# Optimization experiments

Hardware: AMD Instinct MI355X
Metric: run time of the kernel (lower is better)

The kernel has to match this reference:

```python
import jax, jax.numpy as jnp
import numpy as np


def setup_inputs() -> dict:
    key = jax.random.key(0)
    N, D = 8192, 16384  # tokens x latent dim
    inputs = jax.random.normal(key, (N, D), dtype=jnp.float32)
    return {"inputs": inputs, "k": 64}


def reference(inputs, k):
    # top-k along last axis, then scatter values into a zero tensor
    values, indices = jax.lax.top_k(inputs, k)          # [N, k]
    rows = jnp.arange(inputs.shape[0])[:, None]          # [N, 1]
    sparse = jnp.zeros_like(inputs).at[rows, indices].set(values)
    return sparse
```

## Files before the change

kernel.cpp:

```cpp
#include <hip/hip_runtime.h>

#define BLOCK 256
#define ROW_D 16384
#define VPT (ROW_D / (BLOCK * 4))

__device__ __forceinline__ unsigned keyOf(float f) {
    unsigned u = __float_as_uint(f);
    return (u & 0x80000000u) ? ~u : (u | 0x80000000u);
}
__device__ __forceinline__ float valOf(unsigned m) {
    unsigned u = (m & 0x80000000u) ? (m & 0x7FFFFFFFu) : ~m;
    return __uint_as_float(u);
}

__global__ __launch_bounds__(BLOCK, 4)
void TopKActivation_68324339745162_kernel(const float* __restrict__ in,
                                          float* __restrict__ out,
                                          const int* __restrict__ kptr) {
    __shared__ unsigned hist[256 * 32];
    __shared__ unsigned S[256];
    __shared__ unsigned sDigit, sGreater, sBinCnt, sBase;

    const int t = threadIdx.x;
    const unsigned cpy = (unsigned)t & 31u;
    const size_t rowOff = (size_t)blockIdx.x * (size_t)ROW_D;
    const float4* inRow = reinterpret_cast<const float4*>(in + rowOff);
    float4* outRow = reinterpret_cast<float4*>(out + rowOff);

    uint4 keys[VPT];
#pragma unroll
    for (int j = 0; j < VPT; ++j) {
        float4 v = inRow[t + BLOCK * j];
        keys[j].x = keyOf(v.x);
        keys[j].y = keyOf(v.y);
        keys[j].z = keyOf(v.z);
        keys[j].w = keyOf(v.w);
    }

    unsigned rank = (unsigned)(*kptr);
    unsigned prefix = 0u, pmask = 0u;

    for (int pass = 0; pass < 4; ++pass) {
        const int shift = 24 - 8 * pass;
        for (int i = t; i < 256 * 32; i += BLOCK) hist[i] = 0u;
        __syncthreads();
#pragma unroll
        for (int j = 0; j < VPT; ++j) {
            unsigned kk;
            kk = keys[j].x;
            if ((kk & pmask) == prefix) atomicAdd(&hist[(((kk >> shift) & 255u) << 5) | cpy], 1u);
            kk = keys[j].y;
            if ((kk & pmask) == prefix) atomicAdd(&hist[(((kk >> shift) & 255u) << 5) | cpy], 1u);
            kk = keys[j].z;
            if ((kk & pmask) == prefix) atomicAdd(&hist[(((kk >> shift) & 255u) << 5) | cpy], 1u);
            kk = keys[j].w;
            if ((kk & pmask) == prefix) atomicAdd(&hist[(((kk >> shift) & 255u) << 5) | cpy], 1u);
        }
        __syncthreads();
        unsigned c = 0u;
#pragma unroll
        for (int i = 0; i < 32; ++i) c += hist[((unsigned)t << 5) | (unsigned)((t + i) & 31)];
        S[t] = c;
        __syncthreads();
        for (int step = 1; step < 256; step <<= 1) {
            unsigned v = (t + step < 256) ? S[t + step] : 0u;
            __syncthreads();
            c += v;
            S[t] = c;
            __syncthreads();
        }
        unsigned Snext = (t < 255) ? S[t + 1] : 0u;
        if (c >= rank && Snext < rank) {
            sDigit   = (unsigned)t;
            sGreater = Snext;
            sBinCnt  = c - Snext;
        }
        __syncthreads();
        rank -= sGreater;
        prefix |= sDigit << shift;
        pmask  |= 255u << shift;
    }

    const unsigned T = prefix;
    const unsigned need = rank;
    const bool fastTies = (sBinCnt == need);

    if (fastTies) {
#pragma unroll
        for (int j = 0; j < VPT; ++j) {
            float4 o;
            o.x = (keys[j].x >= T) ? valOf(keys[j].x) : 0.0f;
            o.y = (keys[j].y >= T) ? valOf(keys[j].y) : 0.0f;
            o.z = (keys[j].z >= T) ? valOf(keys[j].z) : 0.0f;
            o.w = (keys[j].w >= T) ? valOf(keys[j].w) : 0.0f;
            outRow[t + BLOCK * j] = o;
        }
    } else {
        if (t == 0) sBase = 0u;
        for (int j = 0; j < VPT; ++j) {
            unsigned lc = (unsigned)(keys[j].x == T) + (unsigned)(keys[j].y == T) +
                          (unsigned)(keys[j].z == T) + (unsigned)(keys[j].w == T);
            __syncthreads();
            S[t] = lc;
            __syncthreads();
            unsigned run = lc;
            for (int step = 1; step < 256; step <<= 1) {
                unsigned v = (t >= step) ? S[t - step] : 0u;
                __syncthreads();
                run += v;
                S[t] = run;
                __syncthreads();
            }
            unsigned r = run - lc + sBase;
            float4 o;
            {
                unsigned kk = keys[j].x;
                if (kk > T) o.x = valOf(kk);
                else if (kk == T) { o.x = (r < need) ? valOf(kk) : 0.0f; ++r; }
                else o.x = 0.0f;
            }
            {
                unsigned kk = keys[j].y;
                if (kk > T) o.y = valOf(kk);
                else if (kk == T) { o.y = (r < need) ? valOf(kk) : 0.0f; ++r; }
                else o.y = 0.0f;
            }
            {
                unsigned kk = keys[j].z;
                if (kk > T) o.z = valOf(kk);
                else if (kk == T) { o.z = (r < need) ? valOf(kk) : 0.0f; ++r; }
                else o.z = 0.0f;
            }
            {
                unsigned kk = keys[j].w;
                if (kk > T) o.w = valOf(kk);
                else if (kk == T) { o.w = (r < need) ? valOf(kk) : 0.0f; ++r; }
                else o.w = 0.0f;
            }
            outRow[t + BLOCK * j] = o;
            __syncthreads();
            if (t == BLOCK - 1) sBase += run;
        }
    }
}

extern "C" void kernel_launch(void* const* d_in, const int* in_sizes, int n_in,
                              void* d_out, int out_size, void* d_ws, size_t ws_size,
                              hipStream_t stream) {
    const float* in = (const float*)d_in[0];
    const int* kptr = (const int*)d_in[1];
    float* out = (float*)d_out;
    const int N = in_sizes[0] / ROW_D;
    TopKActivation_68324339745162_kernel<<<dim3(N), dim3(BLOCK), 0, stream>>>(in, out, kptr);
}
```

Before: 890.5 us.

## Prefilter top-k candidates by per-thread max threshold, shrink histogram copies, wave-level scan

```diff
diff --git a/kernel.cpp b/kernel.cpp
--- a/kernel.cpp
+++ b/kernel.cpp
@@ -3,6 +3,8 @@
 #define BLOCK 256
 #define ROW_D 16384
 #define VPT (ROW_D / (BLOCK * 4))
+#define NC 8
+#define CAP 4096
 
 __device__ __forceinline__ unsigned keyOf(float f) {
     unsigned u = __float_as_uint(f);
@@ -11,23 +13,47 @@
 __device__ __forceinline__ float valOf(unsigned m) {
     unsigned u = (m & 0x80000000u) ? (m & 0x7FFFFFFFu) : ~m;
     return __uint_as_float(u);
+}
+
+__device__ __forceinline__ void waveFind(const unsigned* S, unsigned rank, int l,
+                                         unsigned* dDigit, unsigned* dGreater,
+                                         unsigned* dBinCnt) {
+    uint4 h = *reinterpret_cast<const uint4*>(S + 4 * l);
+    unsigned s3 = h.w;
+    unsigned s2 = h.z + s3;
+    unsigned s1 = h.y + s2;
+    unsigned s0 = h.x + s1;
+    unsigned inc = s0;
+#pragma unroll
+    for (int off = 1; off < 64; off <<= 1) {
+        unsigned v = __shfl_down(inc, off);
+        if (l + off < 64) inc += v;
+    }
+    const unsigned E = inc - s0;
+    const unsigned su0 = s0 + E, su1 = s1 + E, su2 = s2 + E, su3 = s3 + E, su4 = E;
+    if (su0 >= rank && su1 < rank) { *dDigit = 4u * l + 0u; *dGreater = su1; *dBinCnt = su0 - su1; }
+    if (su1 >= rank && su2 < rank) { *dDigit = 4u * l + 1u; *dGreater = su2; *dBinCnt = su1 - su2; }
+    if (su2 >= rank && su3 < rank) { *dDigit = 4u * l + 2u; *dGreater = su3; *dBinCnt = su2 - su3; }
+    if (su3 >= rank && su4 < rank) { *dDigit = 4u * l + 3u; *dGreater = su4; *dBinCnt = su3 - su4; }
 }
 
 __global__ __launch_bounds__(BLOCK, 4)
 void TopKActivation_68324339745162_kernel(const float* __restrict__ in,
                                           float* __restrict__ out,
                                           const int* __restrict__ kptr) {
-    __shared__ unsigned hist[256 * 32];
-    __shared__ unsigned S[256];
-    __shared__ unsigned sDigit, sGreater, sBinCnt, sBase;
+    __shared__ unsigned hist[256 * NC];
+    __shared__ __align__(16) unsigned S[256];
+    __shared__ unsigned cand[CAP];
+    __shared__ unsigned sDigit, sGreater, sBinCnt, sCnt, sBase;
 
     const int t = threadIdx.x;
-    const unsigned cpy = (unsigned)t & 31u;
+    const unsigned cpy = (unsigned)t & (NC - 1u);
     const size_t rowOff = (size_t)blockIdx.x * (size_t)ROW_D;
     const float4* inRow = reinterpret_cast<const float4*>(in + rowOff);
     float4* outRow = reinterpret_cast<float4*>(out + rowOff);
 
     uint4 keys[VPT];
+    unsigned mx = 0u;
 #pragma unroll
     for (int j = 0; j < VPT; ++j) {
         float4 v = inRow[t + BLOCK * j];
@@ -35,50 +61,81 @@
         keys[j].y = keyOf(v.y);
         keys[j].z = keyOf(v.z);
         keys[j].w = keyOf(v.w);
-    }
-
-    unsigned rank = (unsigned)(*kptr);
-    unsigned prefix = 0u, pmask = 0u;
-
+        unsigned a = keys[j].x > keys[j].y ? keys[j].x : keys[j].y;
+        unsigned b = keys[j].z > keys[j].w ? keys[j].z : keys[j].w;
+        a = a > b ? a : b;
+        mx = mx > a ? mx : a;
+    }
+
+    const unsigned k0 = (unsigned)(*kptr);
+    const bool screenOK = (k0 >= 1u && k0 <= (unsigned)BLOCK);
+
+    for (int i = t; i < 256 * NC; i += BLOCK) hist[i] = 0u;
+    if (t == 0) sCnt = 0u;
+    __syncthreads();
+    atomicAdd(&hist[((mx >> 24) << 3) | cpy], 1u);
+    __syncthreads();
+    {
+        unsigned s = 0u;
+#pragma unroll
+        for (int c = 0; c < NC; ++c)
+            s += hist[((unsigned)t << 3) | (((unsigned)t + (unsigned)c) & (NC - 1u))];
+        S[t] = s;
+    }
+    __syncthreads();
+    if (t < 64) waveFind(S, screenOK ? k0 : 256u, t, &sDigit, &sGreater, &sBinCnt);
+    __syncthreads();
+    const unsigned Lkey = sDigit << 24;
+
+    if (screenOK) {
+#pragma unroll
+        for (int j = 0; j < VPT; ++j) {
+            unsigned kk;
+            kk = keys[j].x; if (kk >= Lkey) { unsigned p = atomicAdd(&sCnt, 1u); if (p < CAP) cand[p] = kk; }
+            kk = keys[j].y; if (kk >= Lkey) { unsigned p = atomicAdd(&sCnt, 1u); if (p < CAP) cand[p] = kk; }
+            kk = keys[j].z; if (kk >= Lkey) { unsigned p = atomicAdd(&sCnt, 1u); if (p < CAP) cand[p] = kk; }
+            kk = keys[j].w; if (kk >= Lkey) { unsigned p = atomicAdd(&sCnt, 1u); if (p < CAP) cand[p] = kk; }
+        }
+    }
+    __syncthreads();
+    const unsigned M = sCnt;
+    const bool useCand = screenOK && (M <= (unsigned)CAP);
+
+    unsigned rank = k0, prefix = 0u, pmask = 0u;
     for (int pass = 0; pass < 4; ++pass) {
         const int shift = 24 - 8 * pass;
-        for (int i = t; i < 256 * 32; i += BLOCK) hist[i] = 0u;
-        __syncthreads();
-#pragma unroll
-        for (int j = 0; j < VPT; ++j) {
-            unsigned kk;
-            kk = keys[j].x;
-            if ((kk & pmask) == prefix) atomicAdd(&hist[(((kk >> shift) & 255u) << 5) | cpy], 1u);
-            kk = keys[j].y;
-            if ((kk & pmask) == prefix) atomicAdd(&hist[(((kk >> shift) & 255u) << 5) | cpy], 1u);
-            kk = keys[j].z;
-            if ((kk & pmask) == prefix) atomicAdd(&hist[(((kk >> shift) & 255u) << 5) | cpy], 1u);
-            kk = keys[j].w;
-            if ((kk & pmask) == prefix) atomicAdd(&hist[(((kk >> shift) & 255u) << 5) | cpy], 1u);
-        }
-        __syncthreads();
-        unsigned c = 0u;
-#pragma unroll
-        for (int i = 0; i < 32; ++i) c += hist[((unsigned)t << 5) | (unsigned)((t + i) & 31)];
-        S[t] = c;
-        __syncthreads();
-        for (int step = 1; step < 256; step <<= 1) {
-            unsigned v = (t + step < 256) ? S[t + step] : 0u;
-            __syncthreads();
-            c += v;
-            S[t] = c;
-            __syncthreads();
-        }
-        unsigned Snext = (t < 255) ? S[t + 1] : 0u;
-        if (c >= rank && Snext < rank) {
-            sDigit   = (unsigned)t;
-            sGreater = Snext;
-            sBinCnt  = c - Snext;
-        }
+        for (int i = t; i < 256 * NC; i += BLOCK) hist[i] = 0u;
+        __syncthreads();
+        if (useCand) {
+            for (unsigned i = (unsigned)t; i < M; i += BLOCK) {
+                unsigned ck = cand[i];
+                if ((ck & pmask) == prefix)
+                    atomicAdd(&hist[(((ck >> shift) & 255u) << 3) | cpy], 1u);
+            }
+        } else {
+#pragma unroll
+            for (int j = 0; j < VPT; ++j) {
+                unsigned kk;
+                kk = keys[j].x; if ((kk & pmask) == prefix) atomicAdd(&hist[(((kk >> shift) & 255u) << 3) | cpy], 1u);
+                kk = keys[j].y; if ((kk & pmask) == prefix) atomicAdd(&hist[(((kk >> shift) & 255u) << 3) | cpy], 1u);
+                kk = keys[j].z; if ((kk & pmask) == prefix) atomicAdd(&hist[(((kk >> shift) & 255u) << 3) | cpy], 1u);
+                kk = keys[j].w; if ((kk & pmask) == prefix) atomicAdd(&hist[(((kk >> shift) & 255u) << 3) | cpy], 1u);
+            }
+        }
+        __syncthreads();
+        {
+            unsigned s = 0u;
+#pragma unroll
+            for (int c = 0; c < NC; ++c)
+                s += hist[((unsigned)t << 3) | (((unsigned)t + (unsigned)c) & (NC - 1u))];
+            S[t] = s;
+        }
+        __syncthreads();
+        if (t < 64) waveFind(S, rank, t, &sDigit, &sGreater, &sBinCnt);
         __syncthreads();
         rank -= sGreater;
         prefix |= sDigit << shift;
-        pmask  |= 255u << shift;
+        pmask |= 255u << shift;
     }
 
     const unsigned T = prefix;
```

Result: no change. 879.1 us (-1.3%).
